# Optimization experiments

Hardware: AMD Instinct MI355X
Metric: run time of the kernel (lower is better)

## Reference

```python
import jax, jax.numpy as jnp
import numpy as np

N_NODES = 100000
N_EDGES = 1600000
IN_CH = 64
OUT_CH = 64
EDGE_DIM = 32


def setup_inputs() -> dict:
    key = jax.random.key(0)
    ks = jax.random.split(key, 8)
    cat_dim = 2 * IN_CH + EDGE_DIM  # 160
    x = jax.random.normal(ks[0], (N_NODES, IN_CH), dtype=jnp.float32)
    edge_index = jax.random.randint(ks[1], (2, N_EDGES), 0, N_NODES, dtype=jnp.int64)
    edge_attr = jax.random.normal(ks[2], (N_EDGES, EDGE_DIM), dtype=jnp.float32)
    # linear1: (2*in + edge_dim) -> out ; stored as [in, out] for x @ W
    W1 = jax.random.normal(ks[3], (cat_dim, OUT_CH), dtype=jnp.float32) / np.sqrt(cat_dim)
    b1 = jnp.zeros((OUT_CH,), dtype=jnp.float32)
    gamma = jnp.ones((OUT_CH,), dtype=jnp.float32)
    beta = jnp.zeros((OUT_CH,), dtype=jnp.float32)
    W2 = jax.random.normal(ks[4], (OUT_CH, OUT_CH), dtype=jnp.float32) / np.sqrt(OUT_CH)
    b2 = jnp.zeros((OUT_CH,), dtype=jnp.float32)
    return {"x": x, "edge_index": edge_index, "edge_attr": edge_attr,
            "W1": W1, "b1": b1, "gamma": gamma, "beta": beta, "W2": W2, "b2": b2}


def _layer_norm(h, gamma, beta, eps=1e-5):
    mu = jnp.mean(h, axis=-1, keepdims=True)
    var = jnp.var(h, axis=-1, keepdims=True)
    return (h - mu) * jax.lax.rsqrt(var + eps) * gamma + beta


def reference(x, edge_index, edge_attr, W1, b1, gamma, beta, W2, b2):
    i, j = edge_index[0], edge_index[1]
    # gather source/target node features and concat with edge features: [E, 2*in+edge_dim]
    feats = jnp.concatenate([x[i], x[j], edge_attr], axis=-1)
    h = feats @ W1 + b1                       # [E, out]
    h = jax.nn.gelu(_layer_norm(h, gamma, beta), approximate=False)
    m = h @ W2 + b2                           # [E, out]
    # scatter-add messages onto target nodes j, dim_size = N
    return jax.ops.segment_sum(m, j, num_segments=x.shape[0])
```

## Files before the change

### kernel.cpp

```cpp
#include <hip/hip_runtime.h>
#include <math.h>


using short8 = __attribute__((ext_vector_type(8))) short;
using f32x4  = __attribute__((ext_vector_type(4))) float;

#define LDH 72

static __device__ __forceinline__ short f2bf(float f) {
    unsigned u = __float_as_uint(f);
    u += 0x7FFFu + ((u >> 16) & 1u);
    return (short)(u >> 16);
}

static __device__ __forceinline__ short8 pack8(float4 a, float4 b) {
    short8 r;
    r[0] = f2bf(a.x); r[1] = f2bf(a.y); r[2] = f2bf(a.z); r[3] = f2bf(a.w);
    r[4] = f2bf(b.x); r[5] = f2bf(b.y); r[6] = f2bf(b.z); r[7] = f2bf(b.w);
    return r;
}

__global__ void prep_weights(const float* __restrict__ W1,
                             const float* __restrict__ W2,
                             short* __restrict__ Wt1,
                             short* __restrict__ Wt2)
{
    int t = blockIdx.x * blockDim.x + threadIdx.x;
    if (t < 160 * 64) {
        int k = t / 64, n = t % 64;
        Wt1[n * 160 + k] = f2bf(W1[t]);
    }
    int t2 = t - 160 * 64;
    if (t2 >= 0 && t2 < 64 * 64) {
        int k = t2 / 64, n = t2 % 64;
        Wt2[n * 64 + k] = f2bf(W2[t2]);
    }
}

__global__ void prep_x_bf16(const float* __restrict__ x,
                            short* __restrict__ xbf,
                            int total8)
{
    int t = blockIdx.x * blockDim.x + threadIdx.x;
    if (t < total8) {
        const float4* xf4 = (const float4*)x;
        float4 a = xf4[2 * t];
        float4 b = xf4[2 * t + 1];
        ((short8*)xbf)[t] = pack8(a, b);
    }
}

template <bool XBF>
__global__ __launch_bounds__(256) void mpconv_mfma(
    const float* __restrict__ x,
    const short* __restrict__ xbf,
    const int*   __restrict__ ei,
    const float* __restrict__ ea,
    const short* __restrict__ Wt1,
    const float* __restrict__ b1,
    const float* __restrict__ gam,
    const float* __restrict__ bet,
    const short* __restrict__ Wt2,
    const float* __restrict__ b2,
    float*       __restrict__ out,
    int E)
{
    __shared__ __align__(16) short Hlds[4][64][LDH];

    const int wave = threadIdx.x >> 6;
    const int lane = threadIdx.x & 63;
    const int g    = lane >> 4;
    const int col  = lane & 15;
    const int eb   = blockIdx.x * 256 + wave * 64;

    int aedge[4], ii[4], jj[4];
#pragma unroll
    for (int mt = 0; mt < 4; mt++) {
        int e = eb + mt * 16 + col;
        e = (e < E) ? e : (E - 1);
        aedge[mt] = e;
        ii[mt] = ei[e];
        jj[mt] = ei[E + e];
    }

    float b1c[4], gc[4], bc[4], b2c[4];
#pragma unroll
    for (int nt = 0; nt < 4; nt++) {
        int c = col + 16 * nt;
        b1c[nt] = b1[c]; gc[nt] = gam[c]; bc[nt] = bet[c]; b2c[nt] = b2[c];
    }

    f32x4 acc[4][4];
#pragma unroll
    for (int mt = 0; mt < 4; mt++)
#pragma unroll
        for (int nt = 0; nt < 4; nt++)
            acc[mt][nt] = (f32x4){0.f, 0.f, 0.f, 0.f};

#pragma unroll
    for (int ks = 0; ks < 5; ks++) {
        const int k0 = ks * 32;
        const int kk = k0 + g * 8;

        short8 afrag[4];
#pragma unroll
        for (int mt = 0; mt < 4; mt++) {
            if (XBF && k0 < 64) {
                afrag[mt] = *(const short8*)(xbf + (size_t)ii[mt] * 64 + kk);
            } else if (XBF && k0 < 128) {
                afrag[mt] = *(const short8*)(xbf + (size_t)jj[mt] * 64 + (kk - 64));
            } else {
                const float* s;
                if (k0 < 64)       s = x  + (size_t)ii[mt] * 64 + kk;
                else if (k0 < 128) s = x  + (size_t)jj[mt] * 64 + (kk - 64);
                else               s = ea + (size_t)aedge[mt] * 32 + (kk - 128);
                float4 a = *(const float4*)s;
                float4 b = *(const float4*)(s + 4);
                afrag[mt] = pack8(a, b);
            }
        }
        short8 bfrag[4];
#pragma unroll
        for (int nt = 0; nt < 4; nt++)
            bfrag[nt] = *(const short8*)(Wt1 + (size_t)(col + 16 * nt) * 160 + kk);

#pragma unroll
        for (int mt = 0; mt < 4; mt++)
#pragma unroll
            for (int nt = 0; nt < 4; nt++)
                acc[mt][nt] = __builtin_amdgcn_mfma_f32_16x16x32_bf16(
                    afrag[mt], bfrag[nt], acc[mt][nt], 0, 0, 0);
    }

#pragma unroll
    for (int mt = 0; mt < 4; mt++) {
        float s[4] = {0.f, 0.f, 0.f, 0.f};
        float q[4] = {0.f, 0.f, 0.f, 0.f};
#pragma unroll
        for (int nt = 0; nt < 4; nt++) {
#pragma unroll
            for (int r = 0; r < 4; r++) {
                float v = acc[mt][nt][r] + b1c[nt];
                acc[mt][nt][r] = v;
                s[r] += v;
                q[r] += v * v;
            }
        }
#pragma unroll
        for (int m = 1; m < 16; m <<= 1) {
#pragma unroll
            for (int r = 0; r < 4; r++) {
                s[r] += __shfl_xor(s[r], m);
                q[r] += __shfl_xor(q[r], m);
            }
        }
#pragma unroll
        for (int r = 0; r < 4; r++) {
            float mu  = s[r] * (1.0f / 64.0f);
            float var = q[r] * (1.0f / 64.0f) - mu * mu;
            float inv = rsqrtf(var + 1e-5f);
            int row = mt * 16 + g * 4 + r;
#pragma unroll
            for (int nt = 0; nt < 4; nt++) {
                float h = (acc[mt][nt][r] - mu) * inv * gc[nt] + bc[nt];
                h = 0.5f * h * (1.0f + erff(h * 0.70710678118654752f));
                Hlds[wave][row][col + 16 * nt] = f2bf(h);
            }
        }
    }
    __syncthreads();

    f32x4 acc2[4][4];
#pragma unroll
    for (int mt = 0; mt < 4; mt++)
#pragma unroll
        for (int nt = 0; nt < 4; nt++)
            acc2[mt][nt] = (f32x4){0.f, 0.f, 0.f, 0.f};

#pragma unroll
    for (int ks = 0; ks < 2; ks++) {
        const int kk = ks * 32 + g * 8;
        short8 af[4], bf[4];
#pragma unroll
        for (int mt = 0; mt < 4; mt++)
            af[mt] = *(const short8*)&Hlds[wave][mt * 16 + col][kk];
#pragma unroll
        for (int nt = 0; nt < 4; nt++)
            bf[nt] = *(const short8*)(Wt2 + (size_t)(col + 16 * nt) * 64 + kk);
#pragma unroll
        for (int mt = 0; mt < 4; mt++)
#pragma unroll
            for (int nt = 0; nt < 4; nt++)
                acc2[mt][nt] = __builtin_amdgcn_mfma_f32_16x16x32_bf16(
                    af[mt], bf[nt], acc2[mt][nt], 0, 0, 0);
    }

#pragma unroll
    for (int mt = 0; mt < 4; mt++) {
#pragma unroll
        for (int r = 0; r < 4; r++) {
            int e = eb + mt * 16 + g * 4 + r;
            if (e < E) {
                int dst = ei[E + e];
                float* op = out + (size_t)dst * 64 + col;
#pragma unroll
                for (int nt = 0; nt < 4; nt++)
                    unsafeAtomicAdd(op + 16 * nt, acc2[mt][nt][r] + b2c[nt]);
            }
        }
    }
}

extern "C" void kernel_launch(void* const* d_in, const int* in_sizes, int n_in,
                              void* d_out, int out_size, void* d_ws, size_t ws_size,
                              hipStream_t stream)
{
    const float* x   = (const float*)d_in[0];
    const int*   ei  = (const int*)  d_in[1];
    const float* ea  = (const float*)d_in[2];
    const float* W1  = (const float*)d_in[3];
    const float* b1  = (const float*)d_in[4];
    const float* gam = (const float*)d_in[5];
    const float* bet = (const float*)d_in[6];
    const float* W2  = (const float*)d_in[7];
    const float* b2  = (const float*)d_in[8];
    float* out = (float*)d_out;

    const int E = in_sizes[1] / 2;
    const int N = in_sizes[0] / 64;

    short* Wt1 = (short*)d_ws;
    short* Wt2 = Wt1 + 160 * 64;
    const size_t wbytes = (size_t)(160 * 64 + 64 * 64) * sizeof(short);
    short* xbf = (short*)((char*)d_ws + wbytes);
    const size_t need = wbytes + (size_t)N * 64 * sizeof(short);
    const bool use_xbf = (ws_size >= need);

    hipMemsetAsync(d_out, 0, (size_t)out_size * sizeof(float), stream);

    {
        int total = 160 * 64 + 64 * 64;
        int grid = (total + 255) / 256;
        hipLaunchKernelGGL(prep_weights, dim3(grid), dim3(256), 0, stream,
                           W1, W2, Wt1, Wt2);
    }
    if (use_xbf) {
        int total8 = N * 8;
        int grid = (total8 + 255) / 256;
        hipLaunchKernelGGL(prep_x_bf16, dim3(grid), dim3(256), 0, stream,
                           x, xbf, total8);
    }
    {
        int grid = (E + 255) / 256;
        if (use_xbf)
            hipLaunchKernelGGL(mpconv_mfma<true>, dim3(grid), dim3(256), 0, stream,
                               x, xbf, ei, ea, Wt1, b1, gam, bet, Wt2, b2, out, E);
        else
            hipLaunchKernelGGL(mpconv_mfma<false>, dim3(grid), dim3(256), 0, stream,
                               x, xbf, ei, ea, Wt1, b1, gam, bet, Wt2, b2, out, E);
    }
}
```

Before: 691.0 us.

## Sort edges by destination to combine scatter atomics per wave

Adds a counting sort of edges by destination node (histogram, single-block scan, permutation build) and processes edges in sorted order. Each wave stages its output messages in LDS and accumulates runs of equal destination per lane before issuing one atomic per run and channel. This is meant to cut the per-edge-per-channel global atomic traffic. In exchange it adds three preprocessing kernels, a serial single-block scan, and makes edge_attr and edge_index reads indirect through the permutation.

```diff
diff --git a/kernel.cpp b/kernel.cpp
--- a/kernel.cpp
+++ b/kernel.cpp
@@ -6,6 +6,8 @@
 using f32x4  = __attribute__((ext_vector_type(4))) float;
 
 #define LDH 72
+#define WREG 9472
+#define SMEM_BYTES (4 * WREG)
 
 static __device__ __forceinline__ short f2bf(float f) {
     unsigned u = __float_as_uint(f);
@@ -50,7 +52,46 @@
     }
 }
 
-template <bool XBF>
+__global__ void hist_dst(const int* __restrict__ ei, int* __restrict__ counts, int E)
+{
+    int e = blockIdx.x * blockDim.x + threadIdx.x;
+    if (e < E) atomicAdd(&counts[ei[E + e]], 1);
+}
+
+#define SCAN_T 1024
+__global__ __launch_bounds__(SCAN_T) void scan_offsets(const int* __restrict__ counts,
+                                                       int* __restrict__ offs, int N)
+{
+    __shared__ int part[SCAN_T];
+    int t = threadIdx.x;
+    int chunk = (N + SCAN_T - 1) / SCAN_T;
+    int lo = t * chunk, hi = min(lo + chunk, N);
+    int s = 0;
+    for (int i = lo; i < hi; i++) s += counts[i];
+    part[t] = s;
+    __syncthreads();
+    for (int d = 1; d < SCAN_T; d <<= 1) {
+        int v = (t >= d) ? part[t - d] : 0;
+        __syncthreads();
+        part[t] += v;
+        __syncthreads();
+    }
+    int excl = (t == 0) ? 0 : part[t - 1];
+    for (int i = lo; i < hi; i++) { int c = counts[i]; offs[i] = excl; excl += c; }
+}
+
+__global__ void build_perm(const int* __restrict__ ei, int* __restrict__ offs,
+                           int* __restrict__ perm, int E)
+{
+    int e = blockIdx.x * blockDim.x + threadIdx.x;
+    if (e < E) {
+        int dst = ei[E + e];
+        int pos = atomicAdd(&offs[dst], 1);
+        perm[pos] = e;
+    }
+}
+
+template <int MODE>
 __global__ __launch_bounds__(256) void mpconv_mfma(
     const float* __restrict__ x,
     const short* __restrict__ xbf,
@@ -62,10 +103,11 @@
     const float* __restrict__ bet,
     const short* __restrict__ Wt2,
     const float* __restrict__ b2,
+    const int*   __restrict__ perm,
     float*       __restrict__ out,
     int E)
 {
-    __shared__ __align__(16) short Hlds[4][64][LDH];
+    __shared__ __align__(16) char smem[SMEM_BYTES];
 
     const int wave = threadIdx.x >> 6;
     const int lane = threadIdx.x & 63;
@@ -73,14 +115,22 @@
     const int col  = lane & 15;
     const int eb   = blockIdx.x * 256 + wave * 64;
 
+    char* wbase = smem + wave * WREG;
+    short (*Hl)[LDH] = (short (*)[LDH])wbase;
+    float (*Hf)[66]  = (float (*)[66])wbase;
+    int*  dstL       = (int*)(wbase + 9216);
+
     int aedge[4], ii[4], jj[4];
 #pragma unroll
     for (int mt = 0; mt < 4; mt++) {
-        int e = eb + mt * 16 + col;
-        e = (e < E) ? e : (E - 1);
+        int ep = eb + mt * 16 + col;
+        bool v = (ep < E);
+        int epc = v ? ep : (E - 1);
+        int e = (MODE == 2) ? perm[epc] : epc;
         aedge[mt] = e;
         ii[mt] = ei[e];
         jj[mt] = ei[E + e];
+        if (MODE == 2 && g == 0) dstL[mt * 16 + col] = v ? jj[mt] : -1;
     }
 
     float b1c[4], gc[4], bc[4], b2c[4];
@@ -105,9 +155,9 @@
         short8 afrag[4];
 #pragma unroll
         for (int mt = 0; mt < 4; mt++) {
-            if (XBF && k0 < 64) {
+            if (MODE >= 1 && k0 < 64) {
                 afrag[mt] = *(const short8*)(xbf + (size_t)ii[mt] * 64 + kk);
-            } else if (XBF && k0 < 128) {
+            } else if (MODE >= 1 && k0 < 128) {
                 afrag[mt] = *(const short8*)(xbf + (size_t)jj[mt] * 64 + (kk - 64));
             } else {
                 const float* s;
@@ -164,11 +214,10 @@
             for (int nt = 0; nt < 4; nt++) {
                 float h = (acc[mt][nt][r] - mu) * inv * gc[nt] + bc[nt];
                 h = 0.5f * h * (1.0f + erff(h * 0.70710678118654752f));
-                Hlds[wave][row][col + 16 * nt] = f2bf(h);
-            }
-        }
-    }
-    __syncthreads();
+                Hl[row][col + 16 * nt] = f2bf(h);
+            }
+        }
+    }
 
     f32x4 acc2[4][4];
 #pragma unroll
@@ -183,7 +232,7 @@
         short8 af[4], bf[4];
 #pragma unroll
         for (int mt = 0; mt < 4; mt++)
-            af[mt] = *(const short8*)&Hlds[wave][mt * 16 + col][kk];
+            af[mt] = *(const short8*)&Hl[mt * 16 + col][kk];
 #pragma unroll
         for (int nt = 0; nt < 4; nt++)
             bf[nt] = *(const short8*)(Wt2 + (size_t)(col + 16 * nt) * 64 + kk);
@@ -195,17 +244,48 @@
                     af[mt], bf[nt], acc2[mt][nt], 0, 0, 0);
     }
 
-#pragma unroll
-    for (int mt = 0; mt < 4; mt++) {
-#pragma unroll
-        for (int r = 0; r < 4; r++) {
-            int e = eb + mt * 16 + g * 4 + r;
-            if (e < E) {
-                int dst = ei[E + e];
-                float* op = out + (size_t)dst * 64 + col;
+    if (MODE == 2) {
+        int cur = -1;
+        float sum = 0.f;
+#pragma unroll
+        for (int p = 0; p < 2; p++) {
+#pragma unroll
+            for (int m2 = 0; m2 < 2; m2++) {
+                int mt = 2 * p + m2;
 #pragma unroll
                 for (int nt = 0; nt < 4; nt++)
-                    unsafeAtomicAdd(op + 16 * nt, acc2[mt][nt][r] + b2c[nt]);
+#pragma unroll
+                    for (int r = 0; r < 4; r++)
+                        Hf[m2 * 16 + g * 4 + r][col + 16 * nt] =
+                            acc2[mt][nt][r] + b2c[nt];
+            }
+#pragma unroll 4
+            for (int row = 0; row < 32; row++) {
+                int d = dstL[p * 32 + row];
+                float v = Hf[row][lane];
+                if (d != cur) {
+                    if (cur >= 0)
+                        unsafeAtomicAdd(out + (size_t)cur * 64 + lane, sum);
+                    cur = d; sum = 0.f;
+                }
+                if (d >= 0) sum += v;
+            }
+        }
+        if (cur >= 0)
+            unsafeAtomicAdd(out + (size_t)cur * 64 + lane, sum);
+    } else {
+#pragma unroll
+        for (int mt = 0; mt < 4; mt++) {
+#pragma unroll
+            for (int r = 0; r < 4; r++) {
+                int e = eb + mt * 16 + g * 4 + r;
+                if (e < E) {
+                    int dst = ei[E + e];
+                    float* op = out + (size_t)dst * 64 + col;
+#pragma unroll
+                    for (int nt = 0; nt < 4; nt++)
+                        unsafeAtomicAdd(op + 16 * nt, acc2[mt][nt][r] + b2c[nt]);
+                }
             }
         }
     }
@@ -231,10 +311,16 @@
 
     short* Wt1 = (short*)d_ws;
     short* Wt2 = Wt1 + 160 * 64;
-    const size_t wbytes = (size_t)(160 * 64 + 64 * 64) * sizeof(short);
-    short* xbf = (short*)((char*)d_ws + wbytes);
-    const size_t need = wbytes + (size_t)N * 64 * sizeof(short);
-    const bool use_xbf = (ws_size >= need);
+    const size_t woff = (size_t)(160 * 64 + 64 * 64) * sizeof(short);
+    short* xbf = (short*)((char*)d_ws + woff);
+    const size_t need_xbf = woff + (size_t)N * 64 * sizeof(short);
+    const size_t soff = (need_xbf + 255) & ~(size_t)255;
+    int* counts = (int*)((char*)d_ws + soff);
+    int* offs   = counts + N;
+    int* perm   = offs + N;
+    const size_t need_sort = soff + (size_t)N * 8 + (size_t)E * 4;
+
+    const int mode = (ws_size >= need_sort) ? 2 : (ws_size >= need_xbf ? 1 : 0);
 
     hipMemsetAsync(d_out, 0, (size_t)out_size * sizeof(float), stream);
 
@@ -244,19 +330,32 @@
         hipLaunchKernelGGL(prep_weights, dim3(grid), dim3(256), 0, stream,
                            W1, W2, Wt1, Wt2);
     }
-    if (use_xbf) {
+    if (mode >= 1) {
         int total8 = N * 8;
         int grid = (total8 + 255) / 256;
         hipLaunchKernelGGL(prep_x_bf16, dim3(grid), dim3(256), 0, stream,
                            x, xbf, total8);
     }
+    if (mode == 2) {
+        hipMemsetAsync(counts, 0, (size_t)N * sizeof(int), stream);
+        int gridE = (E + 255) / 256;
+        hipLaunchKernelGGL(hist_dst, dim3(gridE), dim3(256), 0, stream,
+                           ei, counts, E);
+        hipLaunchKernelGGL(scan_offsets, dim3(1), dim3(SCAN_T), 0, stream,
+                           counts, offs, N);
+        hipLaunchKernelGGL(build_perm, dim3(gridE), dim3(256), 0, stream,
+                           ei, offs, perm, E);
+    }
     {
         int grid = (E + 255) / 256;
-        if (use_xbf)
-            hipLaunchKernelGGL(mpconv_mfma<true>, dim3(grid), dim3(256), 0, stream,
-                               x, xbf, ei, ea, Wt1, b1, gam, bet, Wt2, b2, out, E);
+        if (mode == 2)
+            hipLaunchKernelGGL(mpconv_mfma<2>, dim3(grid), dim3(256), 0, stream,
+                               x, xbf, ei, ea, Wt1, b1, gam, bet, Wt2, b2, perm, out, E);
+        else if (mode == 1)
+            hipLaunchKernelGGL(mpconv_mfma<1>, dim3(grid), dim3(256), 0, stream,
+                               x, xbf, ei, ea, Wt1, b1, gam, bet, Wt2, b2, perm, out, E);
         else
-            hipLaunchKernelGGL(mpconv_mfma<false>, dim3(grid), dim3(256), 0, stream,
-                               x, xbf, ei, ea, Wt1, b1, gam, bet, Wt2, b2, out, E);
-    }
-}
+            hipLaunchKernelGGL(mpconv_mfma<0>, dim3(grid), dim3(256), 0, stream,
+                               x, xbf, ei, ea, Wt1, b1, gam, bet, Wt2, b2, perm, out, E);
+    }
+}
```

Result: slower. 934.8 us (+35.3%).
